# Performance work log

Measured on AMD Instinct MI355X. Metric: run time of the kernel, lower is better.

The kernel has to match this reference:

```python
import jax, jax.numpy as jnp
import numpy as np

B, T, D = 1, 4096, 2048
H = 16
D_NOPE, D_ROPE, D_V = 128, 64, 128
D_QK = D_NOPE + D_ROPE          # 192
KV_RANK = 512
SCALE = D_QK ** -0.5
EPS = 1e-5
ROPE_BASE = 10000.0


def _rope_tables(T, d):
    inv_freq = 1.0 / (ROPE_BASE ** (jnp.arange(0, d, 2, dtype=jnp.float32) / d))
    ang = jnp.arange(T, dtype=jnp.float32)[:, None] * inv_freq[None, :]  # [T, d/2]
    return jnp.cos(ang), jnp.sin(ang)


def _apply_rope(x, cos, sin):
    # x: [..., d]; cos/sin broadcastable to [..., d/2]; interleaved pairs
    x1, x2 = x[..., 0::2], x[..., 1::2]
    out = jnp.stack([x1 * cos - x2 * sin, x1 * sin + x2 * cos], axis=-1)
    return out.reshape(x.shape)


def _layernorm(x, g, b):
    mu = jnp.mean(x, axis=-1, keepdims=True)
    var = jnp.var(x, axis=-1, keepdims=True)
    return (x - mu) * jax.lax.rsqrt(var + EPS) * g + b


def setup_inputs() -> dict:
    key = jax.random.key(0)
    ks = jax.random.split(key, 6)
    s = 0.02
    return {
        "x": jax.random.normal(ks[0], (B, T, D), jnp.float32),
        "wq": jax.random.normal(ks[1], (H * D_QK, D), jnp.float32) * s,
        "wkv_a": jax.random.normal(ks[2], (KV_RANK + D_ROPE, D), jnp.float32) * s,
        "kv_gamma": jnp.ones((KV_RANK,), jnp.float32),
        "kv_beta": jnp.zeros((KV_RANK,), jnp.float32),
        "wkv_b": jax.random.normal(ks[3], (H * (D_NOPE + D_V), KV_RANK), jnp.float32) * s,
        "wo": jax.random.normal(ks[4], (D, H * D_V), jnp.float32) * s,
    }


def reference(x, wq, wkv_a, kv_gamma, kv_beta, wkv_b, wo):
    # Query projection (q_lora_rank == 0 path): [B,T,H,D_QK]
    q = (x @ wq.T).reshape(B, T, H, D_QK)
    q_nope, q_pe = q[..., :D_NOPE], q[..., D_NOPE:]

    # Low-rank KV projection: kv latent [B,T,KV_RANK], shared rope key [B,T,D_ROPE]
    kv_full = x @ wkv_a.T
    kv, k_pe = kv_full[..., :KV_RANK], kv_full[..., KV_RANK:]

    cos, sin = _rope_tables(T, D_ROPE)  # [T, D_ROPE/2]
    q_pe = _apply_rope(q_pe, cos[None, :, None, :], sin[None, :, None, :])
    k_pe = _apply_rope(k_pe, cos[None, :, :], sin[None, :, :])

    # Up-project normalized latent to per-head nope-keys and values
    kv = _layernorm(kv, kv_gamma, kv_beta)
    kvb = (kv @ wkv_b.T).reshape(B, T, H, D_NOPE + D_V)
    k_nope, v = kvb[..., :D_NOPE], kvb[..., D_NOPE:]

    # Scores: nope part per head + rope part with shared k_pe
    scores = (
        jnp.einsum("bshd,bthd->bhst", q_nope, k_nope)
        + jnp.einsum("bshd,btd->bhst", q_pe, k_pe)
    ) * SCALE

    causal = jnp.tril(jnp.ones((T, T), bool))
    scores = jnp.where(causal[None, None], scores, -jnp.inf)
    probs = jax.nn.softmax(scores, axis=-1)

    out = jnp.einsum("bhst,bthd->bshd", probs, v).reshape(B, T, H * D_V)
    return out @ wo.T
```

## Files before the change

### kernel.cpp

```cpp
#include <hip/hip_runtime.h>
#include <hip/hip_bf16.h>

typedef __attribute__((ext_vector_type(8))) short bf16x8;
typedef __attribute__((ext_vector_type(4))) float f32x4;
typedef __attribute__((address_space(3))) unsigned int lds_u32;
typedef __attribute__((address_space(1))) const unsigned int glb_u32;

#define LOG2_10000 13.287712379549449f
#define QSCALE (0.07216878364870323f * 1.4426950408889634f)

static __device__ __forceinline__ unsigned short f2bf(float f) {
  union { float f; unsigned int u; } v; v.f = f;
  unsigned int r = v.u + 0x7FFFu + ((v.u >> 16) & 1u);
  return (unsigned short)(r >> 16);
}
static __device__ __forceinline__ float bf2f(unsigned short h) {
  union { unsigned int u; float f; } v; v.u = ((unsigned int)h) << 16;
  return v.f;
}
static __device__ __forceinline__ f32x4 mfma16(bf16x8 a, bf16x8 b, f32x4 c) {
  return __builtin_amdgcn_mfma_f32_16x16x32_bf16(a, b, c, 0, 0, 0);
}
static __device__ __forceinline__ void gl_lds16(const void* g, void* l) {
  __builtin_amdgcn_global_load_lds((glb_u32*)g, (lds_u32*)l, 16, 0, 0);
}

__global__ __launch_bounds__(256) void cast_bf16(const float* __restrict__ src,
                                                 unsigned short* __restrict__ dst,
                                                 int nsrc, int ndst) {
  int i = (blockIdx.x * 256 + threadIdx.x) * 4;
  if (i >= ndst) return;
  float4 v = make_float4(0.f, 0.f, 0.f, 0.f);
  if (i < nsrc) v = *(const float4*)(src + i);
  uint2 o;
  o.x = (unsigned int)f2bf(v.x) | ((unsigned int)f2bf(v.y) << 16);
  o.y = (unsigned int)f2bf(v.z) | ((unsigned int)f2bf(v.w) << 16);
  *(uint2*)(dst + i) = o;
}

template <bool OUTBF>
__global__ __launch_bounds__(256, 2) void gemm_bf16(const unsigned short* __restrict__ A,
                                                    const unsigned short* __restrict__ Bt,
                                                    void* __restrict__ Cv,
                                                    int M, int N, int K, float alpha) {
  __shared__ unsigned short As[128 * 32];
  __shared__ unsigned short Bs[128 * 32];
  const int tid = threadIdx.x;
  const int w = tid >> 6, lane = tid & 63;
  const int quad = lane >> 4, l15 = lane & 15;
  const int wx = w & 1, wy = w >> 1;
  const int bm = blockIdx.y * 128, bn = blockIdx.x * 128;

  f32x4 acc[4][4];
#pragma unroll
  for (int i = 0; i < 4; ++i)
#pragma unroll
    for (int j = 0; j < 4; ++j) { acc[i][j][0] = 0.f; acc[i][j][1] = 0.f; acc[i][j][2] = 0.f; acc[i][j][3] = 0.f; }

  const int lrow = lane >> 2;
  const int lcol = (lane & 3) * 8;
  const unsigned short* Ag = A + (size_t)(bm + w * 16 + lrow) * K + lcol;
  const unsigned short* Bg = Bt + (size_t)(bn + w * 16 + lrow) * K + lcol;
  unsigned short* AsB = &As[(w * 16) * 32];
  unsigned short* BsB = &Bs[(w * 16) * 32];

  for (int k0 = 0; k0 < K; k0 += 32) {
    __syncthreads();
    gl_lds16(Ag + k0, AsB);
    gl_lds16(Ag + (size_t)64 * K + k0, AsB + 64 * 32);
    gl_lds16(Bg + k0, BsB);
    gl_lds16(Bg + (size_t)64 * K + k0, BsB + 64 * 32);
    __syncthreads();
    bf16x8 aF[4], bF[4];
#pragma unroll
    for (int i = 0; i < 4; ++i)
      aF[i] = *(const bf16x8*)&As[(wy * 64 + i * 16 + l15) * 32 + quad * 8];
#pragma unroll
    for (int j = 0; j < 4; ++j)
      bF[j] = *(const bf16x8*)&Bs[(wx * 64 + j * 16 + l15) * 32 + quad * 8];
#pragma unroll
    for (int i = 0; i < 4; ++i)
#pragma unroll
      for (int j = 0; j < 4; ++j)
        acc[i][j] = mfma16(aF[i], bF[j], acc[i][j]);
  }

#pragma unroll
  for (int i = 0; i < 4; ++i)
#pragma unroll
    for (int r = 0; r < 4; ++r) {
      const size_t row = (size_t)(bm + wy * 64 + i * 16 + quad * 4 + r) * (size_t)N;
#pragma unroll
      for (int j = 0; j < 4; ++j) {
        const int col = bn + wx * 64 + j * 16 + l15;
        if (OUTBF) ((unsigned short*)Cv)[row + col] = f2bf(acc[i][j][r] * alpha);
        else       ((float*)Cv)[row + col] = acc[i][j][r];
      }
    }
}

__global__ __launch_bounds__(256) void rope_q_bf(unsigned short* __restrict__ qh) {
  int idx = blockIdx.x * 256 + threadIdx.x;
  int j = idx & 31;
  int th = idx >> 5;
  int h = th & 15;
  int t = th >> 4;
  float fr = exp2f(-(float)j * (LOG2_10000 / 32.f));
  float ang = (float)t * fr;
  float sn, cs;
  sincosf(ang, &sn, &cs);
  unsigned short* p = qh + (size_t)t * 3072 + h * 192 + 128 + 2 * j;
  unsigned int v = *(unsigned int*)p;
  float a = bf2f((unsigned short)v), b = bf2f((unsigned short)(v >> 16));
  float na = a * cs - b * sn, nb = a * sn + b * cs;
  *(unsigned int*)p = (unsigned int)f2bf(na) | ((unsigned int)f2bf(nb) << 16);
}

__global__ __launch_bounds__(256) void ln_rope_k(const float* __restrict__ kvfull,
                                                 const float* __restrict__ gamma,
                                                 const float* __restrict__ beta,
                                                 unsigned short* __restrict__ kvln,
                                                 unsigned short* __restrict__ kpe) {
  const int t = blockIdx.x;
  const int tid = threadIdx.x;
  const float* row = kvfull + (size_t)t * 640;
  float x0 = row[tid], x1 = row[tid + 256];
  float sm = x0 + x1;
  float sq = x0 * x0 + x1 * x1;
#pragma unroll
  for (int off = 1; off < 64; off <<= 1) {
    sm += __shfl_xor(sm, off, 64);
    sq += __shfl_xor(sq, off, 64);
  }
  __shared__ float rs[4], rq[4];
  const int lane = tid & 63, wid = tid >> 6;
  if (lane == 0) { rs[wid] = sm; rq[wid] = sq; }
  __syncthreads();
  float tsm = rs[0] + rs[1] + rs[2] + rs[3];
  float tsq = rq[0] + rq[1] + rq[2] + rq[3];
  float mu = tsm * (1.f / 512.f);
  float var = tsq * (1.f / 512.f) - mu * mu;
  float inv = rsqrtf(var + 1e-5f);
  kvln[(size_t)t * 512 + tid]       = f2bf((x0 - mu) * inv * gamma[tid] + beta[tid]);
  kvln[(size_t)t * 512 + tid + 256] = f2bf((x1 - mu) * inv * gamma[tid + 256] + beta[tid + 256]);
  if (tid < 32) {
    float a = row[512 + 2 * tid], b = row[512 + 2 * tid + 1];
    float fr = exp2f(-(float)tid * (LOG2_10000 / 32.f));
    float ang = (float)t * fr;
    float sn, cs;
    sincosf(ang, &sn, &cs);
    kpe[(size_t)t * 64 + 2 * tid]     = f2bf(a * cs - b * sn);
    kpe[(size_t)t * 64 + 2 * tid + 1] = f2bf(a * sn + b * cs);
  }
}

__global__ __launch_bounds__(256) void transpose_v(const unsigned short* __restrict__ kvb,
                                                   unsigned short* __restrict__ Vt) {
  __shared__ unsigned short tile[64][72];
  const int tb = blockIdx.x * 64;
  const int h  = blockIdx.y >> 1;
  const int c0 = (blockIdx.y & 1) * 64;
  const int tid = threadIdx.x;
  const int r  = tid >> 4;
  const int c4 = (tid & 15) * 4;
#pragma unroll
  for (int rep = 0; rep < 4; ++rep) {
    const int t = rep * 16 + r;
    uint2 d = *(const uint2*)(kvb + (size_t)(tb + t) * 4096 + h * 256 + 128 + c0 + c4);
    *(uint2*)&tile[t][c4] = d;
  }
  __syncthreads();
#pragma unroll
  for (int rep = 0; rep < 4; ++rep) {
    const int c = rep * 16 + r;
    unsigned int lo = (unsigned int)tile[c4 + 0][c] | ((unsigned int)tile[c4 + 1][c] << 16);
    unsigned int hi = (unsigned int)tile[c4 + 2][c] | ((unsigned int)tile[c4 + 3][c] << 16);
    uint2 o; o.x = lo; o.y = hi;
    *(uint2*)(Vt + ((size_t)h * 128 + c0 + c) * 4096 + tb + c4) = o;
  }
}

__global__ __launch_bounds__(256, 2) void attn_mfma(const unsigned short* __restrict__ qh,
                                                    const unsigned short* __restrict__ kvb,
                                                    const unsigned short* __restrict__ kpe,
                                                    const unsigned short* __restrict__ Vt,
                                                    unsigned short* __restrict__ attnh) {
  __shared__ unsigned short sK[3 * 4096];
  __shared__ unsigned short sVt[128 * 64];
  __shared__ unsigned short sP[128 * 72];

  const int bid = blockIdx.x;
  const int h = bid & 15;
  const int z = bid >> 4;
  const int qt = (z < 16) ? (31 - z) : (z - 16);
  const int q0 = qt * 128;
  const int tid = threadIdx.x;
  const int w = tid >> 6, lane = tid & 63;
  const int quad = lane >> 4, l15 = lane & 15;
  const int wq0 = w * 32;

  const unsigned short* kvbh = kvb + h * 256;
  const unsigned short* Vth = Vt + (size_t)h * 128 * 4096;

  bf16x8 qF[2][6];
#pragma unroll
  for (int i = 0; i < 2; ++i)
#pragma unroll
    for (int g = 0; g < 6; ++g) {
      const int grow = q0 + wq0 + i * 16 + l15;
      union { uint4 u; bf16x8 v; } tmp;
      tmp.u = *(const uint4*)(qh + (size_t)grow * 3072 + h * 192 + g * 32 + quad * 8);
      qF[i][g] = tmp.v;
    }

  f32x4 oA[2][8];
  float mi[2], li[2];
#pragma unroll
  for (int i = 0; i < 2; ++i) {
    mi[i] = -1e30f; li[i] = 0.f;
#pragma unroll
    for (int j = 0; j < 8; ++j) { oA[i][j][0] = 0.f; oA[i][j][1] = 0.f; oA[i][j][2] = 0.f; oA[i][j][3] = 0.f; }
  }

  const int nk = 2 * (qt + 1);
  for (int kt = 0; kt < nk; ++kt) {
    const int k0 = kt * 64;
    __syncthreads();

#pragma unroll
    for (int j = 0; j < 6; ++j) {
      const int i = w * 6 + j;
      const int granule = i * 64 + lane;
      const int sp = granule >> 9;
      const int t = granule & 511;
      const int key = t >> 3;
      const int c = t & 7;
      const int c_src = c ^ (key & 7);
      const int col = (sp << 6) + (c_src << 3);
      const unsigned short* src = (sp < 2)
          ? kvbh + (size_t)(k0 + key) * 4096 + col
          : kpe + (size_t)(k0 + key) * 64 + (col - 128);
      gl_lds16(src, &sK[i * 512]);
    }
#pragma unroll
    for (int j = 0; j < 4; ++j) {
      const int ii = w * 4 + j;
      const int n = ii * 8 + (lane >> 3);
      const int b = (lane & 7) ^ ((lane >> 3) & 7);
      gl_lds16(Vth + (size_t)n * 4096 + k0 + b * 8, &sVt[ii * 512]);
    }
    __syncthreads();

    f32x4 sc[4][2];
#pragma unroll
    for (int kk = 0; kk < 4; ++kk)
#pragma unroll
      for (int i = 0; i < 2; ++i) { sc[kk][i][0] = 0.f; sc[kk][i][1] = 0.f; sc[kk][i][2] = 0.f; sc[kk][i][3] = 0.f; }
#pragma unroll
    for (int g = 0; g < 6; ++g) {
      const int sp = g >> 1;
      const int cbase = (g & 1) * 4;
      bf16x8 kF[4];
#pragma unroll
      for (int kk = 0; kk < 4; ++kk) {
        const int row = kk * 16 + l15;
        const int cc = (cbase + quad) ^ (l15 & 7);
        kF[kk] = *(const bf16x8*)&sK[sp * 4096 + row * 64 + cc * 8];
      }
#pragma unroll
      for (int kk = 0; kk < 4; ++kk)
#pragma unroll
        for (int i = 0; i < 2; ++i)
          sc[kk][i] = mfma16(kF[kk], qF[i][g], sc[kk][i]);
    }

    const bool msk = (kt >= 2 * qt);
    float alpha[2];
#pragma unroll
    for (int i = 0; i < 2; ++i) {
      const int grow = q0 + wq0 + i * 16 + l15;
      if (msk) {
#pragma unroll
        for (int kk = 0; kk < 4; ++kk)
#pragma unroll
          for (int rr = 0; rr < 4; ++rr) {
            const int gk = k0 + kk * 16 + quad * 4 + rr;
            if (gk > grow) sc[kk][i][rr] = -1e30f;
          }
      }
      float t0 = fmaxf(fmaxf(sc[0][i][0], sc[0][i][1]), fmaxf(sc[0][i][2], sc[0][i][3]));
      float t1 = fmaxf(fmaxf(sc[1][i][0], sc[1][i][1]), fmaxf(sc[1][i][2], sc[1][i][3]));
      float t2 = fmaxf(fmaxf(sc[2][i][0], sc[2][i][1]), fmaxf(sc[2][i][2], sc[2][i][3]));
      float t3 = fmaxf(fmaxf(sc[3][i][0], sc[3][i][1]), fmaxf(sc[3][i][2], sc[3][i][3]));
      float mx = fmaxf(fmaxf(t0, t1), fmaxf(t2, t3));
      mx = fmaxf(mx, __shfl_xor(mx, 16, 64));
      mx = fmaxf(mx, __shfl_xor(mx, 32, 64));
      const float mnew = fmaxf(mi[i], mx);
      alpha[i] = __builtin_amdgcn_exp2f(mi[i] - mnew);
#pragma unroll
      for (int kk = 0; kk < 4; ++kk)
#pragma unroll
        for (int rr = 0; rr < 4; ++rr)
          sc[kk][i][rr] = __builtin_amdgcn_exp2f(sc[kk][i][rr] - mnew);
      float s0 = (sc[0][i][0] + sc[0][i][1]) + (sc[0][i][2] + sc[0][i][3]);
      float s1 = (sc[1][i][0] + sc[1][i][1]) + (sc[1][i][2] + sc[1][i][3]);
      float s2 = (sc[2][i][0] + sc[2][i][1]) + (sc[2][i][2] + sc[2][i][3]);
      float s3 = (sc[3][i][0] + sc[3][i][1]) + (sc[3][i][2] + sc[3][i][3]);
      float sum = (s0 + s1) + (s2 + s3);
      sum += __shfl_xor(sum, 16, 64);
      sum += __shfl_xor(sum, 32, 64);
      li[i] = li[i] * alpha[i] + sum;
      mi[i] = mnew;
    }

#pragma unroll
    for (int i = 0; i < 2; ++i) {
      if (__any(alpha[i] < 1.f)) {
#pragma unroll
        for (int rr = 0; rr < 4; ++rr) {
          const float af = __shfl(alpha[i], (lane & 48) | (quad * 4 + rr), 64);
#pragma unroll
          for (int j = 0; j < 8; ++j) oA[i][j][rr] *= af;
        }
      }
    }

#pragma unroll
    for (int kk = 0; kk < 4; ++kk)
#pragma unroll
      for (int i = 0; i < 2; ++i) {
        union { float f; unsigned int u; } p0, p1, p2, p3;
        p0.f = sc[kk][i][0]; p1.f = sc[kk][i][1]; p2.f = sc[kk][i][2]; p3.f = sc[kk][i][3];
        uint2 pk;
        pk.x = (p0.u >> 16) | (p1.u & 0xFFFF0000u);
        pk.y = (p2.u >> 16) | (p3.u & 0xFFFF0000u);
        *(uint2*)&sP[(size_t)(wq0 + i * 16 + l15) * 72 + kk * 16 + quad * 4] = pk;
      }

#pragma unroll
    for (int ks = 0; ks < 2; ++ks) {
      bf16x8 pF[2], vF[8];
#pragma unroll
      for (int i = 0; i < 2; ++i)
        pF[i] = *(const bf16x8*)&sP[(size_t)(wq0 + i * 16 + l15) * 72 + ks * 32 + quad * 8];
#pragma unroll
      for (int j = 0; j < 8; ++j) {
        const int n = j * 16 + l15;
        const int blk = (ks * 4 + quad) ^ (l15 & 7);
        vF[j] = *(const bf16x8*)&sVt[(size_t)n * 64 + blk * 8];
      }
#pragma unroll
      for (int i = 0; i < 2; ++i)
#pragma unroll
        for (int j = 0; j < 8; ++j)
          oA[i][j] = mfma16(pF[i], vF[j], oA[i][j]);
    }
  }

  float linv[2];
  linv[0] = 1.f / li[0];
  linv[1] = 1.f / li[1];
#pragma unroll
  for (int i = 0; i < 2; ++i)
#pragma unroll
    for (int rr = 0; rr < 4; ++rr) {
      const float lf = __shfl(linv[i], (lane & 48) | (quad * 4 + rr), 64);
      const size_t grow = (size_t)(q0 + wq0 + i * 16 + quad * 4 + rr);
#pragma unroll
      for (int j = 0; j < 8; ++j)
        attnh[grow * 2048 + h * 128 + j * 16 + l15] = f2bf(oA[i][j][rr] * lf);
    }
}

extern "C" void kernel_launch(void* const* d_in, const int* in_sizes, int n_in,
                              void* d_out, int out_size, void* d_ws, size_t ws_size,
                              hipStream_t stream) {
  const float* x        = (const float*)d_in[0];
  const float* wq       = (const float*)d_in[1];
  const float* wkv_a    = (const float*)d_in[2];
  const float* kv_gamma = (const float*)d_in[3];
  const float* kv_beta  = (const float*)d_in[4];
  const float* wkv_b    = (const float*)d_in[5];
  const float* wo       = (const float*)d_in[6];
  float* out = (float*)d_out;

  char* p = (char*)d_ws;
  unsigned short* xh    = (unsigned short*)p; p += (size_t)4096 * 2048 * 2;
  unsigned short* wqh   = (unsigned short*)p; p += (size_t)3072 * 2048 * 2;
  unsigned short* wah   = (unsigned short*)p; p += (size_t)640 * 2048 * 2;
  unsigned short* wbh   = (unsigned short*)p; p += (size_t)4096 * 512 * 2;
  unsigned short* woh   = (unsigned short*)p; p += (size_t)2048 * 2048 * 2;
  unsigned short* qh    = (unsigned short*)p; p += (size_t)4096 * 3072 * 2;
  float*          kvful = (float*)p;          p += (size_t)4096 * 640 * 4;
  unsigned short* kvlnh = (unsigned short*)p; p += (size_t)4096 * 512 * 2;
  unsigned short* kpeh  = (unsigned short*)p; p += (size_t)4096 * 64 * 2;
  unsigned short* kvbh  = (unsigned short*)p; p += (size_t)4096 * 4096 * 2;
  unsigned short* attnh = (unsigned short*)p; p += (size_t)4096 * 2048 * 2;
  if ((size_t)(p - (char*)d_ws) > ws_size) return;
  unsigned short* Vt = xh;

  cast_bf16<<<8192, 256, 0, stream>>>(x,     xh,  4096 * 2048, 4096 * 2048);
  cast_bf16<<<6144, 256, 0, stream>>>(wq,    wqh, 3072 * 2048, 3072 * 2048);
  cast_bf16<<<1280, 256, 0, stream>>>(wkv_a, wah, 576 * 2048,  640 * 2048);
  cast_bf16<<<2048, 256, 0, stream>>>(wkv_b, wbh, 4096 * 512,  4096 * 512);
  cast_bf16<<<4096, 256, 0, stream>>>(wo,    woh, 2048 * 2048, 2048 * 2048);

  gemm_bf16<true><<<dim3(24, 32), 256, 0, stream>>>(xh, wqh, qh, 4096, 3072, 2048, QSCALE);
  rope_q_bf<<<8192, 256, 0, stream>>>(qh);
  gemm_bf16<false><<<dim3(5, 32), 256, 0, stream>>>(xh, wah, kvful, 4096, 640, 2048, 1.f);
  ln_rope_k<<<4096, 256, 0, stream>>>(kvful, kv_gamma, kv_beta, kvlnh, kpeh);
  gemm_bf16<true><<<dim3(32, 32), 256, 0, stream>>>(kvlnh, wbh, kvbh, 4096, 4096, 512, 1.f);
  transpose_v<<<dim3(64, 32), 256, 0, stream>>>(kvbh, Vt);
  attn_mfma<<<512, 256, 0, stream>>>(qh, kvbh, kpeh, Vt, attnh);
  gemm_bf16<false><<<dim3(16, 32), 256, 0, stream>>>(attnh, woh, out, 4096, 2048, 2048, 1.f);
}
```

Baseline: 486.3 us.

## Double-buffer K/V LDS tiles in attention kernel with async prefetch

Splits the K and V^T shared-memory tiles into two buffers. The next key tile is prefetched via global_load_lds while the current tile is being computed, and explicit vmcnt waits plus barriers replace the per-iteration syncthreads pair. This is meant to hide global-memory latency behind the MFMA work. LDS use roughly doubles, so launch bounds drop from 2 to 1 blocks per SM, which may cut occupancy. The hand-written waitcnt of 10 must match the outstanding load count per wave.

```diff
diff --git a/kernel.cpp b/kernel.cpp
--- a/kernel.cpp
+++ b/kernel.cpp
@@ -180,13 +180,43 @@
   }
 }
 
-__global__ __launch_bounds__(256, 2) void attn_mfma(const unsigned short* __restrict__ qh,
+static __device__ __forceinline__ void stage_kv(const unsigned short* kvbh,
+                                                const unsigned short* kpe,
+                                                const unsigned short* Vth,
+                                                int k0, unsigned short* sKb,
+                                                unsigned short* sVb,
+                                                int w, int lane) {
+#pragma unroll
+  for (int j = 0; j < 6; ++j) {
+    const int i = w * 6 + j;
+    const int granule = i * 64 + lane;
+    const int sp = granule >> 9;
+    const int t = granule & 511;
+    const int key = t >> 3;
+    const int c = t & 7;
+    const int c_src = c ^ (key & 7);
+    const int col = (sp << 6) + (c_src << 3);
+    const unsigned short* src = (sp < 2)
+        ? kvbh + (size_t)(k0 + key) * 4096 + col
+        : kpe + (size_t)(k0 + key) * 64 + (col - 128);
+    gl_lds16(src, sKb + i * 512);
+  }
+#pragma unroll
+  for (int j = 0; j < 4; ++j) {
+    const int ii = w * 4 + j;
+    const int n = ii * 8 + (lane >> 3);
+    const int b = (lane & 7) ^ ((lane >> 3) & 7);
+    gl_lds16(Vth + (size_t)n * 4096 + k0 + b * 8, sVb + ii * 512);
+  }
+}
+
+__global__ __launch_bounds__(256, 1) void attn_mfma(const unsigned short* __restrict__ qh,
                                                     const unsigned short* __restrict__ kvb,
                                                     const unsigned short* __restrict__ kpe,
                                                     const unsigned short* __restrict__ Vt,
                                                     unsigned short* __restrict__ attnh) {
-  __shared__ unsigned short sK[3 * 4096];
-  __shared__ unsigned short sVt[128 * 64];
+  __shared__ unsigned short sK[2][3 * 4096];
+  __shared__ unsigned short sVt[2][128 * 64];
   __shared__ unsigned short sP[128 * 72];
 
   const int bid = blockIdx.x;
@@ -223,33 +253,23 @@
   }
 
   const int nk = 2 * (qt + 1);
+
+  stage_kv(kvbh, kpe, Vth, 0, &sK[0][0], &sVt[0][0], w, lane);
+
   for (int kt = 0; kt < nk; ++kt) {
     const int k0 = kt * 64;
-    __syncthreads();
-
-#pragma unroll
-    for (int j = 0; j < 6; ++j) {
-      const int i = w * 6 + j;
-      const int granule = i * 64 + lane;
-      const int sp = granule >> 9;
-      const int t = granule & 511;
-      const int key = t >> 3;
-      const int c = t & 7;
-      const int c_src = c ^ (key & 7);
-      const int col = (sp << 6) + (c_src << 3);
-      const unsigned short* src = (sp < 2)
-          ? kvbh + (size_t)(k0 + key) * 4096 + col
-          : kpe + (size_t)(k0 + key) * 64 + (col - 128);
-      gl_lds16(src, &sK[i * 512]);
-    }
-#pragma unroll
-    for (int j = 0; j < 4; ++j) {
-      const int ii = w * 4 + j;
-      const int n = ii * 8 + (lane >> 3);
-      const int b = (lane & 7) ^ ((lane >> 3) & 7);
-      gl_lds16(Vth + (size_t)n * 4096 + k0 + b * 8, &sVt[ii * 512]);
-    }
-    __syncthreads();
+    const int cur = kt & 1;
+
+    if (kt + 1 < nk)
+      stage_kv(kvbh, kpe, Vth, k0 + 64, &sK[cur ^ 1][0], &sVt[cur ^ 1][0], w, lane);
+
+    if (kt + 1 < nk) { __asm__ __volatile__("s_waitcnt vmcnt(10)" ::: "memory"); }
+    else             { __asm__ __volatile__("s_waitcnt vmcnt(0)" ::: "memory"); }
+    __builtin_amdgcn_s_barrier();
+    __asm__ __volatile__("" ::: "memory");
+
+    const unsigned short* sKc = &sK[cur][0];
+    const unsigned short* sVc = &sVt[cur][0];
 
     f32x4 sc[4][2];
 #pragma unroll
@@ -265,7 +285,7 @@
       for (int kk = 0; kk < 4; ++kk) {
         const int row = kk * 16 + l15;
         const int cc = (cbase + quad) ^ (l15 & 7);
-        kF[kk] = *(const bf16x8*)&sK[sp * 4096 + row * 64 + cc * 8];
+        kF[kk] = *(const bf16x8*)&sKc[sp * 4096 + row * 64 + cc * 8];
       }
 #pragma unroll
       for (int kk = 0; kk < 4; ++kk)
@@ -347,7 +367,7 @@
       for (int j = 0; j < 8; ++j) {
         const int n = j * 16 + l15;
         const int blk = (ks * 4 + quad) ^ (l15 & 7);
-        vF[j] = *(const bf16x8*)&sVt[(size_t)n * 64 + blk * 8];
+        vF[j] = *(const bf16x8*)&sVc[(size_t)n * 64 + blk * 8];
       }
 #pragma unroll
       for (int i = 0; i < 2; ++i)
@@ -355,6 +375,10 @@
         for (int j = 0; j < 8; ++j)
           oA[i][j] = mfma16(pF[i], vF[j], oA[i][j]);
     }
+
+    __asm__ __volatile__("s_waitcnt lgkmcnt(0)" ::: "memory");
+    __builtin_amdgcn_s_barrier();
+    __asm__ __volatile__("" ::: "memory");
   }
 
   float linv[2];
```

Result: slower. 550.6 us (+13.2%).
